# Performance work log

Measured on AMD Instinct MI355X. Metric: run time of the kernel, lower is better.

Reference implementation:

```python
import jax, jax.numpy as jnp
import numpy as np

B, N, E = 2, 10000, 80000
NODE_DIM, EDGE_DIM = 30, 3
H, VE, EE = 64, 16, 16  # encoder_hidden_dim -> width AND depth of hidden chain


def _mlp_params(key, din, h, dout, prefix):
    k = jax.random.split(key, 6)
    s_in, s_h = 1.0 / np.sqrt(din), 1.0 / np.sqrt(h)
    return {
        prefix + '_Win': jax.random.normal(k[0], (din, h), jnp.float32) * s_in,
        prefix + '_bin': jax.random.normal(k[1], (h,), jnp.float32) * s_in,
        prefix + '_Whid': jax.random.normal(k[2], (h, h, h), jnp.float32) * s_h,  # h stacked hidden Linears
        prefix + '_bhid': jax.random.normal(k[3], (h, h), jnp.float32) * s_h,
        prefix + '_Wout': jax.random.normal(k[4], (h, dout), jnp.float32) * s_h,
        prefix + '_bout': jax.random.normal(k[5], (dout,), jnp.float32) * s_h,
    }


def setup_inputs() -> dict:
    key = jax.random.key(0)
    ks = jax.random.split(key, 8)
    inp = {
        'nodes': jax.random.normal(ks[0], (B, N, NODE_DIM), jnp.float32),
        'globals_': jax.random.normal(ks[1], (B,), jnp.float32),
        'edges': jax.random.normal(ks[2], (B, E, EDGE_DIM), jnp.float32),
        'senders': jax.random.randint(ks[3], (B, E), 0, N, jnp.int32),
        'receivers': jax.random.randint(ks[4], (B, E), 0, N, jnp.int32),
    }
    inp.update(_mlp_params(ks[5], NODE_DIM + 1, H, VE, 'node'))  # +1 global col
    inp.update(_mlp_params(ks[6], EDGE_DIM + 4, H, EE, 'edge'))  # +4 relative feats
    return inp


def _chain(x, Win, b_in, Whid, bhid, Wout, bout):
    # Linear(in,h) -> h x Linear(h,h) -> Linear(h,out); NO nonlinearity (matches source)
    h = x @ Win + b_in
    def step(c, wb):
        W, b = wb
        return c @ W + b, None
    h, _ = jax.lax.scan(step, h, (Whid, bhid))
    return h @ Wout + bout


def reference(nodes, globals_, edges, senders, receivers,
              node_Win, node_bin, node_Whid, node_bhid, node_Wout, node_bout,
              edge_Win, edge_bin, edge_Whid, edge_bhid, edge_Wout, edge_bout):
    Bv, Nv = nodes.shape[0], nodes.shape[1]
    g = jnp.broadcast_to(globals_[:, None, None], (Bv, Nv, 1))
    nodes_g = jnp.concatenate([nodes, g], axis=-1)  # [B,N,node_dim+1]
    pos = nodes_g[..., :3]  # first 3 features are 3D positions
    gather = jax.vmap(lambda p, idx: p[idx])
    s = gather(pos, senders)    # [B,E,3]
    r = gather(pos, receivers)  # [B,E,3]
    d = s - r
    norm = jnp.linalg.norm(d, axis=-1, keepdims=True)
    edges_full = jnp.concatenate([edges, d, norm], axis=-1)  # [B,E,edge_dim+4]
    latent_nodes = _chain(nodes_g, node_Win, node_bin, node_Whid, node_bhid, node_Wout, node_bout)
    latent_edges = _chain(edges_full, edge_Win, edge_bin, edge_Whid, edge_bhid, edge_Wout, edge_bout)
    return latent_nodes, latent_edges
```

## Files before the change

### kernel.cpp

```cpp
#include <hip/hip_runtime.h>

typedef unsigned int uint32;

#define NN 10000
#define EE_ 80000
#define NODE_ROWS 20000
#define NODE_BLOCKS 79
#define EDGE_BLOCKS 625

#define FLAG_MAGIC 0x5EEDF00Du
#define FLAG_BASE_U32 640

typedef float f4 __attribute__((ext_vector_type(4)));

#define GLD4(g, l) __builtin_amdgcn_global_load_lds(                      \
    (const __attribute__((address_space(1))) void*)(g),                   \
    (__attribute__((address_space(3))) void*)(l), 16, 0, 0)
#define GLD1(g, l) __builtin_amdgcn_global_load_lds(                      \
    (const __attribute__((address_space(1))) void*)(g),                   \
    (__attribute__((address_space(3))) void*)(l), 4, 0, 0)

__global__ __launch_bounds__(256, 1) void collapse_kernel(
    const float* __restrict__ nWin, const float* __restrict__ nbin,
    const float* __restrict__ nWhid, const float* __restrict__ nbhid,
    const float* __restrict__ nWout, const float* __restrict__ nbout,
    const float* __restrict__ eWin, const float* __restrict__ ebin,
    const float* __restrict__ eWhid, const float* __restrict__ ebhid,
    const float* __restrict__ eWout, const float* __restrict__ ebout,
    float* __restrict__ ws)
{
  __shared__ float smem[13312];
  const int t = threadIdx.x;
  const int c  = blockIdx.x >> 4;
  const int jq = blockIdx.x & 15;
  float* pt = ws + 1024;
  uint32* ws_u = (uint32*)ws;

  {
    float* s_at = smem;
    float* s_b  = smem + 8704;
    float* s_bp = smem + 12864;
    const float* Wh = c ? eWhid : nWhid;
    const float* bh = c ? ebhid : nbhid;
    const int L0 = 4*jq;

    for (int idx = t; idx < 4160; idx += 256) {
      int r = idx >> 6, k = idx & 63;
      s_at[k*68 + r] = (r < 64) ? Wh[(size_t)L0*4096 + idx] : bh[L0*64 + k];
    }
    int cur = 0;
    #pragma unroll 1
    for (int s = 1; s <= 3; ++s) {
      const float* WB = Wh + (size_t)(L0 + s)*4096;
      const float* bB = bh + (size_t)(L0 + s)*64;
      #pragma unroll
      for (int i = 0; i < 4; ++i) {
        int i4 = t + i*256;
        *(float4*)&s_b[i4*4] = *(const float4*)&WB[i4*4];
      }
      if (t < 16) *(float4*)&s_b[4096 + t*4] = *(const float4*)&bB[t*4];
      __syncthreads();

      const int ti = t >> 4, tj = t & 15;
      float acc[4][4];
      #pragma unroll
      for (int d = 0; d < 4; ++d)
        #pragma unroll
        for (int e = 0; e < 4; ++e) acc[d][e] = 0.f;
      #pragma unroll 4
      for (int k = 0; k < 64; ++k) {
        float4 a4 = *(const float4*)&s_at[cur*4352 + k*68 + 4*ti];
        float4 b4 = *(const float4*)&s_b[k*64 + 4*tj];
        float av[4] = {a4.x, a4.y, a4.z, a4.w};
        float bv[4] = {b4.x, b4.y, b4.z, b4.w};
        #pragma unroll
        for (int d = 0; d < 4; ++d)
          #pragma unroll
          for (int e = 0; e < 4; ++e) acc[d][e] += av[d]*bv[e];
      }
      {
        int cc = t & 63, kq = t >> 6;
        float p = 0.f;
        #pragma unroll 4
        for (int kk = 0; kk < 16; ++kk) {
          int k = kq*16 + kk;
          p += s_at[cur*4352 + k*68 + 64] * s_b[k*64 + cc];
        }
        s_bp[kq*64 + cc] = p;
      }
      __syncthreads();
      if (s < 3) {
        #pragma unroll
        for (int d = 0; d < 4; ++d)
          #pragma unroll
          for (int e = 0; e < 4; ++e)
            s_at[(cur^1)*4352 + (4*tj + e)*68 + 4*ti + d] = acc[d][e];
        if (t < 64)
          s_at[(cur^1)*4352 + t*68 + 64] =
              s_bp[t] + s_bp[64+t] + s_bp[128+t] + s_bp[192+t] + s_b[4096+t];
        __syncthreads();
        cur ^= 1;
      } else {
        float* D = pt + (size_t)(c*16 + jq)*4160;
        #pragma unroll
        for (int d = 0; d < 4; ++d)
          *(float4*)&D[(4*ti + d)*64 + 4*tj] =
              make_float4(acc[d][0], acc[d][1], acc[d][2], acc[d][3]);
        if (t < 64)
          D[4096 + t] = s_bp[t] + s_bp[64+t] + s_bp[128+t] + s_bp[192+t] + s_b[4096+t];
      }
    }
  }

  __syncthreads();
  if (t == 0) {
    __threadfence();
    __hip_atomic_store(ws_u + FLAG_BASE_U32 + (c*16 + jq)*8, FLAG_MAGIC,
                       __ATOMIC_RELEASE, __HIP_MEMORY_SCOPE_AGENT);
  }
  if (t < 16) {
    const uint32* p = ws_u + FLAG_BASE_U32 + (c*16 + t)*8;
    int guard = 0;
    while (__hip_atomic_load(p, __ATOMIC_ACQUIRE, __HIP_MEMORY_SCOPE_AGENT)
           != FLAG_MAGIC) {
      __builtin_amdgcn_s_sleep(2);
      if (++guard > (1 << 20)) break;
    }
  }
  __syncthreads();

  {
    float* lds_f = smem;
    const int lane = t & 63;
    const int wv   = __builtin_amdgcn_readfirstlane(t >> 6);
    const int q = jq;
    const float* Win  = c ? eWin  : nWin;
    const float* bin  = c ? ebin  : nbin;
    const float* Wout = c ? eWout : nWout;
    const float* bout = c ? ebout : nbout;
    const float* PT = pt + (size_t)c*16*4160;
    const int din = c ? 7 : 31;
    float* weff = ws + (c ? 512 : 0);

    const int r4 = lane >> 4, c16 = lane & 15;
    const int oE = r4*64 + ((c16 ^ r4) << 2);
    const int oO = r4*64 + ((c16 ^ (4 | r4)) << 2);
    const int swz = lane & 7;
    const int aw0 = lane*256 + (((4*wv + 0) ^ swz) << 4);
    const int aw1 = lane*256 + (((4*wv + 1) ^ swz) << 4);
    const int aw2 = lane*256 + (((4*wv + 2) ^ swz) << 4);
    const int aw3 = lane*256 + (((4*wv + 3) ^ swz) << 4);
    const int ab  = 16384 + wv*256 + lane*4;
    const int apw = 52224 + lane*16 + wv*4;
    const int apr = 52224 + lane*16;

    float vlane = Wout[lane*16 + q];
    float bpart = 0.f;
    const int kbase = 16*wv;
    float s[16];
    #pragma unroll
    for (int j = 0; j < 16; ++j)
      s[j] = __uint_as_float(__builtin_amdgcn_readlane(__float_as_uint(vlane), kbase + j));

#define STAGE(BF, L) do {                                                 \
    const float* gW_ = PT + (size_t)(L)*4160 + wv*1024;                   \
    float* lW_ = lds_f + (BF)*4352 + wv*1024;                             \
    GLD4(gW_ +   0 + oE, lW_ +   0);                                      \
    GLD4(gW_ + 256 + oO, lW_ + 256);                                      \
    GLD4(gW_ + 512 + oE, lW_ + 512);                                      \
    GLD4(gW_ + 768 + oO, lW_ + 768);                                      \
    GLD1(PT + (size_t)(L)*4160 + 4096 + lane,                             \
         lds_f + (BF)*4352 + 4096 + wv*64);                               \
  } while (0)

#define CSTEP(OFS, VMC, STAGESTMT) do {                                   \
    STAGESTMT;                                                            \
    asm volatile("s_waitcnt vmcnt(" #VMC ") lgkmcnt(0)" ::: "memory");    \
    __builtin_amdgcn_s_barrier();                                         \
    f4 f0_, f1_, f2_, f3_; float bb_;                                     \
    asm volatile("ds_read_b128 %0, %5 offset:" #OFS "\n\t"                \
                 "ds_read_b128 %1, %6 offset:" #OFS "\n\t"                \
                 "ds_read_b128 %2, %7 offset:" #OFS "\n\t"                \
                 "ds_read_b128 %3, %8 offset:" #OFS "\n\t"                \
                 "ds_read_b32  %4, %9 offset:" #OFS "\n\t"                \
                 "s_waitcnt lgkmcnt(0)"                                   \
                 : "=&v"(f0_), "=&v"(f1_), "=&v"(f2_), "=&v"(f3_), "=&v"(bb_) \
                 : "v"(aw0), "v"(aw1), "v"(aw2), "v"(aw3), "v"(ab)        \
                 : "memory");                                             \
    __builtin_amdgcn_sched_barrier(0);                                    \
    bpart = __builtin_fmaf(bb_, vlane, bpart);                            \
    float a0_ = __builtin_fmaf(f0_.y, s[1],  f0_.x * s[0]);               \
    a0_ = __builtin_fmaf(f0_.z, s[2],  a0_);                              \
    a0_ = __builtin_fmaf(f0_.w, s[3],  a0_);                              \
    float a1_ = __builtin_fmaf(f1_.y, s[5],  f1_.x * s[4]);               \
    a1_ = __builtin_fmaf(f1_.z, s[6],  a1_);                              \
    a1_ = __builtin_fmaf(f1_.w, s[7],  a1_);                              \
    float a2_ = __builtin_fmaf(f2_.y, s[9],  f2_.x * s[8]);               \
    a2_ = __builtin_fmaf(f2_.z, s[10], a2_);                              \
    a2_ = __builtin_fmaf(f2_.w, s[11], a2_);                              \
    float a3_ = __builtin_fmaf(f3_.y, s[13], f3_.x * s[12]);              \
    a3_ = __builtin_fmaf(f3_.z, s[14], a3_);                              \
    a3_ = __builtin_fmaf(f3_.w, s[15], a3_);                              \
    float acc_ = (a0_ + a1_) + (a2_ + a3_);                               \
    asm volatile("ds_write_b32 %0, %1\n\t"                                \
                 "s_waitcnt lgkmcnt(0)"                                   \
                 :: "v"(apw), "v"(acc_) : "memory");                      \
    __builtin_amdgcn_s_barrier();                                         \
    f4 p4_;                                                               \
    asm volatile("ds_read_b128 %0, %1\n\t"                                \
                 "s_waitcnt lgkmcnt(0)"                                   \
                 : "=&v"(p4_) : "v"(apr) : "memory");                     \
    __builtin_amdgcn_sched_barrier(0);                                    \
    vlane = (p4_.x + p4_.y) + (p4_.z + p4_.w);                            \
    _Pragma("unroll")                                                     \
    for (int jj = 0; jj < 16; ++jj)                                       \
      s[jj] = __uint_as_float(__builtin_amdgcn_readlane(                  \
                  __float_as_uint(vlane), kbase + jj));                   \
  } while (0)

    STAGE(0, 15);
    STAGE(1, 14);

    int L = 15;
    #pragma unroll 1
    for (int ii = 0; ii < 4; ++ii) {
      CSTEP(0,     10, STAGE(2, L-2));
      CSTEP(17408, 10, STAGE(0, L-3));
      CSTEP(34816, 10, STAGE(1, L-4));
      L -= 3;
    }
    CSTEP(0,     10, STAGE(2, 1));
    CSTEP(17408, 10, STAGE(0, 0));
    CSTEP(34816, 5,  (void)0);
    CSTEP(0,     0,  (void)0);
#undef CSTEP
#undef STAGE

    if (wv != 0) return;

    float red = __builtin_fmaf(bin[lane], vlane, bpart);
    #pragma unroll
    for (int off = 32; off > 0; off >>= 1) red += __shfl_xor(red, off, 64);

    float* sv = lds_f;
    sv[lane] = vlane;
    __builtin_amdgcn_sched_barrier(0);

    if (lane == din) {
      weff[din*16 + q] = red + bout[q];
    } else if (lane < din) {
      float a0 = 0.f, a1 = 0.f, a2 = 0.f, a3 = 0.f;
      const float* wr = Win + (size_t)lane*64;
      #pragma unroll
      for (int kb = 0; kb < 16; ++kb) {
        f4 vv = *(const f4*)&sv[kb*4];
        f4 wv4 = *(const f4*)&wr[kb*4];
        a0 = __builtin_fmaf(wv4.x, vv.x, a0);
        a1 = __builtin_fmaf(wv4.y, vv.y, a1);
        a2 = __builtin_fmaf(wv4.z, vv.z, a2);
        a3 = __builtin_fmaf(wv4.w, vv.w, a3);
      }
      weff[lane*16 + q] = (a0 + a1) + (a2 + a3);
    }
  }
}

template<int NF>
static __device__ __forceinline__ void mlp_apply_store(const float* x, const float* sW,
                                                       float* po)
{
  float a[16];
  #pragma unroll
  for (int q = 0; q < 16; ++q) a[q] = sW[NF*16 + q];
  #pragma unroll
  for (int j = 0; j < NF; ++j) {
    const float xv = x[j];
    #pragma unroll
    for (int q = 0; q < 16; ++q) a[q] += xv * sW[j*16 + q];
  }
  float4* d = (float4*)po;
  d[0] = make_float4(a[0],  a[1],  a[2],  a[3]);
  d[1] = make_float4(a[4],  a[5],  a[6],  a[7]);
  d[2] = make_float4(a[8],  a[9],  a[10], a[11]);
  d[3] = make_float4(a[12], a[13], a[14], a[15]);
}

__global__ __launch_bounds__(256) void apply_kernel(
    const float* __restrict__ nodes, const float* __restrict__ globals_,
    const float* __restrict__ edges, const int* __restrict__ senders,
    const int* __restrict__ receivers, const float* __restrict__ ws,
    float* __restrict__ out)
{
  __shared__ float sW[32*16];
  const bool is_node = (blockIdx.x < NODE_BLOCKS);
  {
    const float* src = is_node ? ws : ws + 512;
    const int n = is_node ? 32*16 : 8*16;
    for (int j = threadIdx.x; j < n; j += 256) sW[j] = src[j];
  }
  __syncthreads();

  if (is_node) {
    const int rn = blockIdx.x*256 + threadIdx.x;
    if (rn >= NODE_ROWS) return;
    float x[31];
    const float* p = nodes + (size_t)rn*30;
    #pragma unroll
    for (int j = 0; j < 15; ++j) {
      float2 u = *(const float2*)(p + j*2);
      x[2*j]     = u.x;
      x[2*j + 1] = u.y;
    }
    const int b = (rn >= NN) ? 1 : 0;
    x[30] = globals_[b];
    mlp_apply_store<31>(x, sW, out + (size_t)rn*16);
  } else {
    const int re = (blockIdx.x - NODE_BLOCKS)*256 + threadIdx.x;
    const int b = (re >= EE_) ? 1 : 0;
    float x[7];
    const float* ep = edges + (size_t)re*3;
    x[0] = ep[0]; x[1] = ep[1]; x[2] = ep[2];
    const int si = senders[re], ri = receivers[re];
    const float* ps = nodes + ((size_t)(b*NN + si))*30;
    const float* pr = nodes + ((size_t)(b*NN + ri))*30;
    const float dx = ps[0] - pr[0];
    const float dy = ps[1] - pr[1];
    const float dz = ps[2] - pr[2];
    x[3] = dx; x[4] = dy; x[5] = dz;
    x[6] = sqrtf(dx*dx + dy*dy + dz*dz);
    mlp_apply_store<7>(x, sW, out + (size_t)(NODE_ROWS + re)*16);
  }
}

extern "C" void kernel_launch(void* const* d_in, const int* in_sizes, int n_in,
                              void* d_out, int out_size, void* d_ws, size_t ws_size,
                              hipStream_t stream)
{
  const float* nodes    = (const float*)d_in[0];
  const float* globals_ = (const float*)d_in[1];
  const float* edges    = (const float*)d_in[2];
  const int* senders   = (const int*)d_in[3];
  const int* receivers = (const int*)d_in[4];
  const float* nWin  = (const float*)d_in[5];
  const float* nbin  = (const float*)d_in[6];
  const float* nWhid = (const float*)d_in[7];
  const float* nbhid = (const float*)d_in[8];
  const float* nWout = (const float*)d_in[9];
  const float* nbout = (const float*)d_in[10];
  const float* eWin  = (const float*)d_in[11];
  const float* ebin  = (const float*)d_in[12];
  const float* eWhid = (const float*)d_in[13];
  const float* ebhid = (const float*)d_in[14];
  const float* eWout = (const float*)d_in[15];
  const float* ebout = (const float*)d_in[16];
  float* ws  = (float*)d_ws;
  float* out = (float*)d_out;

  collapse_kernel<<<32, 256, 0, stream>>>(
      nWin, nbin, nWhid, nbhid, nWout, nbout,
      eWin, ebin, eWhid, ebhid, eWout, ebout, ws);

  apply_kernel<<<NODE_BLOCKS + EDGE_BLOCKS, 256, 0, stream>>>(
      nodes, globals_, edges, senders, receivers, ws, out);
}
```

Baseline: 37.63 us.

## Fuse weight-collapse and apply kernels into one flag-synchronized mega kernel

Merges the collapse and apply kernels into a single launch. The first 32 blocks compute the collapsed effective weights and publish per-column and per-chain ready flags. The remaining blocks load their node and edge inputs, including the sender/receiver gathers, before spin-waiting on the flag for their chain. This removes the second launch and its gap, and overlaps input fetching with the weight collapse. In exchange it relies on all blocks being co-resident, since the apply blocks now use the large shared allocation. The flags are never reset, so on repeated calls the apply blocks may not wait and could read weights that are still being rewritten.

```diff
diff --git a/kernel.cpp b/kernel.cpp
--- a/kernel.cpp
+++ b/kernel.cpp
@@ -7,9 +7,14 @@
 #define NODE_ROWS 20000
 #define NODE_BLOCKS 79
 #define EDGE_BLOCKS 625
+#define COLLAPSE_BLOCKS 32
+#define TOTAL_BLOCKS (COLLAPSE_BLOCKS + NODE_BLOCKS + EDGE_BLOCKS)
 
 #define FLAG_MAGIC 0x5EEDF00Du
-#define FLAG_BASE_U32 640
+#define CHUNKFLAG_U32 640
+#define COLFLAG_U32   960
+#define CHAINFLAG_U32 1280
+#define PT_F 2048
 
 typedef float f4 __attribute__((ext_vector_type(4)));
 
@@ -20,21 +25,107 @@
     (const __attribute__((address_space(1))) void*)(g),                   \
     (__attribute__((address_space(3))) void*)(l), 4, 0, 0)
 
-__global__ __launch_bounds__(256, 1) void collapse_kernel(
+template<int NF>
+static __device__ __forceinline__ void mlp_apply_store(const float* x, const float* sW,
+                                                       float* po)
+{
+  float a[16];
+  #pragma unroll
+  for (int q = 0; q < 16; ++q) a[q] = sW[NF*16 + q];
+  #pragma unroll
+  for (int j = 0; j < NF; ++j) {
+    const float xv = x[j];
+    #pragma unroll
+    for (int q = 0; q < 16; ++q) a[q] += xv * sW[j*16 + q];
+  }
+  float4* d = (float4*)po;
+  d[0] = make_float4(a[0],  a[1],  a[2],  a[3]);
+  d[1] = make_float4(a[4],  a[5],  a[6],  a[7]);
+  d[2] = make_float4(a[8],  a[9],  a[10], a[11]);
+  d[3] = make_float4(a[12], a[13], a[14], a[15]);
+}
+
+__global__ __launch_bounds__(256, 1) void mega_kernel(
+    const float* __restrict__ nodes, const float* __restrict__ globals_,
+    const float* __restrict__ edges, const int* __restrict__ senders,
+    const int* __restrict__ receivers,
     const float* __restrict__ nWin, const float* __restrict__ nbin,
     const float* __restrict__ nWhid, const float* __restrict__ nbhid,
     const float* __restrict__ nWout, const float* __restrict__ nbout,
     const float* __restrict__ eWin, const float* __restrict__ ebin,
     const float* __restrict__ eWhid, const float* __restrict__ ebhid,
     const float* __restrict__ eWout, const float* __restrict__ ebout,
-    float* __restrict__ ws)
+    float* __restrict__ ws, float* __restrict__ out)
 {
   __shared__ float smem[13312];
   const int t = threadIdx.x;
+  uint32* ws_u = (uint32*)ws;
+  float* pt = ws + PT_F;
+
+  if (blockIdx.x >= COLLAPSE_BLOCKS) {
+    const int ab = blockIdx.x - COLLAPSE_BLOCKS;
+    const bool is_node = (ab < NODE_BLOCKS);
+    float x[31];
+    int rn = 0, re = 0, b = 0;
+    bool active = true;
+    if (is_node) {
+      rn = ab*256 + t;
+      active = (rn < NODE_ROWS);
+      if (active) {
+        const float* p = nodes + (size_t)rn*30;
+        #pragma unroll
+        for (int j = 0; j < 15; ++j) {
+          float2 u = *(const float2*)(p + j*2);
+          x[2*j]     = u.x;
+          x[2*j + 1] = u.y;
+        }
+        b = (rn >= NN) ? 1 : 0;
+        x[30] = globals_[b];
+      }
+    } else {
+      re = (ab - NODE_BLOCKS)*256 + t;
+      b = (re >= EE_) ? 1 : 0;
+      const float* ep = edges + (size_t)re*3;
+      x[0] = ep[0]; x[1] = ep[1]; x[2] = ep[2];
+      const int si = senders[re], ri = receivers[re];
+      const float* ps = nodes + ((size_t)(b*NN + si))*30;
+      const float* pr = nodes + ((size_t)(b*NN + ri))*30;
+      const float dx = ps[0] - pr[0];
+      const float dy = ps[1] - pr[1];
+      const float dz = ps[2] - pr[2];
+      x[3] = dx; x[4] = dy; x[5] = dz;
+      x[6] = sqrtf(dx*dx + dy*dy + dz*dz);
+    }
+    if (active) {
+      const int nf = is_node ? 31 : 7;
+      #pragma unroll
+      for (int i = 0; i < 31; ++i)
+        if (i < nf) asm volatile("" :: "v"(x[i]));
+    }
+    if (t == 0) {
+      const uint32* p = ws_u + CHAINFLAG_U32 + (is_node ? 0 : 8);
+      int guard = 0;
+      while (__hip_atomic_load(p, __ATOMIC_ACQUIRE, __HIP_MEMORY_SCOPE_AGENT)
+             != FLAG_MAGIC) {
+        __builtin_amdgcn_s_sleep(32);
+        if (++guard > (1 << 16)) break;
+      }
+    }
+    __syncthreads();
+    {
+      const float* src = ws + (is_node ? 0 : 512);
+      const int n = is_node ? 512 : 128;
+      for (int j = t; j < n; j += 256) smem[j] = src[j];
+    }
+    __syncthreads();
+    if (!active) return;
+    if (is_node) mlp_apply_store<31>(x, smem, out + (size_t)rn*16);
+    else         mlp_apply_store<7>(x, smem, out + (size_t)(NODE_ROWS + re)*16);
+    return;
+  }
+
   const int c  = blockIdx.x >> 4;
   const int jq = blockIdx.x & 15;
-  float* pt = ws + 1024;
-  uint32* ws_u = (uint32*)ws;
 
   {
     float* s_at = smem;
@@ -79,14 +170,14 @@
           for (int e = 0; e < 4; ++e) acc[d][e] += av[d]*bv[e];
       }
       {
-        int cc = t & 63, kq = t >> 6;
+        int cc2 = t & 63, kq = t >> 6;
         float p = 0.f;
         #pragma unroll 4
         for (int kk = 0; kk < 16; ++kk) {
           int k = kq*16 + kk;
-          p += s_at[cur*4352 + k*68 + 64] * s_b[k*64 + cc];
+          p += s_at[cur*4352 + k*68 + 64] * s_b[k*64 + cc2];
         }
-        s_bp[kq*64 + cc] = p;
+        s_bp[kq*64 + cc2] = p;
       }
       __syncthreads();
       if (s < 3) {
@@ -115,11 +206,11 @@
   __syncthreads();
   if (t == 0) {
     __threadfence();
-    __hip_atomic_store(ws_u + FLAG_BASE_U32 + (c*16 + jq)*8, FLAG_MAGIC,
+    __hip_atomic_store(ws_u + CHUNKFLAG_U32 + (c*16 + jq)*8, FLAG_MAGIC,
                        __ATOMIC_RELEASE, __HIP_MEMORY_SCOPE_AGENT);
   }
   if (t < 16) {
-    const uint32* p = ws_u + FLAG_BASE_U32 + (c*16 + t)*8;
+    const uint32* p = ws_u + CHUNKFLAG_U32 + (c*16 + t)*8;
     int guard = 0;
     while (__hip_atomic_load(p, __ATOMIC_ACQUIRE, __HIP_MEMORY_SCOPE_AGENT)
            != FLAG_MAGIC) {
@@ -150,7 +241,7 @@
     const int aw1 = lane*256 + (((4*wv + 1) ^ swz) << 4);
     const int aw2 = lane*256 + (((4*wv + 2) ^ swz) << 4);
     const int aw3 = lane*256 + (((4*wv + 3) ^ swz) << 4);
-    const int ab  = 16384 + wv*256 + lane*4;
+    const int ab2 = 16384 + wv*256 + lane*4;
     const int apw = 52224 + lane*16 + wv*4;
     const int apr = 52224 + lane*16;
 
@@ -185,7 +276,7 @@
                  "ds_read_b32  %4, %9 offset:" #OFS "\n\t"                \
                  "s_waitcnt lgkmcnt(0)"                                   \
                  : "=&v"(f0_), "=&v"(f1_), "=&v"(f2_), "=&v"(f3_), "=&v"(bb_) \
-                 : "v"(aw0), "v"(aw1), "v"(aw2), "v"(aw3), "v"(ab)        \
+                 : "v"(aw0), "v"(aw1), "v"(aw2), "v"(aw3), "v"(ab2)       \
                  : "memory");                                             \
     __builtin_amdgcn_sched_barrier(0);                                    \
     bpart = __builtin_fmaf(bb_, vlane, bpart);                            \
@@ -262,73 +353,25 @@
       }
       weff[lane*16 + q] = (a0 + a1) + (a2 + a3);
     }
-  }
-}
-
-template<int NF>
-static __device__ __forceinline__ void mlp_apply_store(const float* x, const float* sW,
-                                                       float* po)
-{
-  float a[16];
-  #pragma unroll
-  for (int q = 0; q < 16; ++q) a[q] = sW[NF*16 + q];
-  #pragma unroll
-  for (int j = 0; j < NF; ++j) {
-    const float xv = x[j];
-    #pragma unroll
-    for (int q = 0; q < 16; ++q) a[q] += xv * sW[j*16 + q];
-  }
-  float4* d = (float4*)po;
-  d[0] = make_float4(a[0],  a[1],  a[2],  a[3]);
-  d[1] = make_float4(a[4],  a[5],  a[6],  a[7]);
-  d[2] = make_float4(a[8],  a[9],  a[10], a[11]);
-  d[3] = make_float4(a[12], a[13], a[14], a[15]);
-}
-
-__global__ __launch_bounds__(256) void apply_kernel(
-    const float* __restrict__ nodes, const float* __restrict__ globals_,
-    const float* __restrict__ edges, const int* __restrict__ senders,
-    const int* __restrict__ receivers, const float* __restrict__ ws,
-    float* __restrict__ out)
-{
-  __shared__ float sW[32*16];
-  const bool is_node = (blockIdx.x < NODE_BLOCKS);
-  {
-    const float* src = is_node ? ws : ws + 512;
-    const int n = is_node ? 32*16 : 8*16;
-    for (int j = threadIdx.x; j < n; j += 256) sW[j] = src[j];
-  }
-  __syncthreads();
-
-  if (is_node) {
-    const int rn = blockIdx.x*256 + threadIdx.x;
-    if (rn >= NODE_ROWS) return;
-    float x[31];
-    const float* p = nodes + (size_t)rn*30;
-    #pragma unroll
-    for (int j = 0; j < 15; ++j) {
-      float2 u = *(const float2*)(p + j*2);
-      x[2*j]     = u.x;
-      x[2*j + 1] = u.y;
-    }
-    const int b = (rn >= NN) ? 1 : 0;
-    x[30] = globals_[b];
-    mlp_apply_store<31>(x, sW, out + (size_t)rn*16);
-  } else {
-    const int re = (blockIdx.x - NODE_BLOCKS)*256 + threadIdx.x;
-    const int b = (re >= EE_) ? 1 : 0;
-    float x[7];
-    const float* ep = edges + (size_t)re*3;
-    x[0] = ep[0]; x[1] = ep[1]; x[2] = ep[2];
-    const int si = senders[re], ri = receivers[re];
-    const float* ps = nodes + ((size_t)(b*NN + si))*30;
-    const float* pr = nodes + ((size_t)(b*NN + ri))*30;
-    const float dx = ps[0] - pr[0];
-    const float dy = ps[1] - pr[1];
-    const float dz = ps[2] - pr[2];
-    x[3] = dx; x[4] = dy; x[5] = dz;
-    x[6] = sqrtf(dx*dx + dy*dy + dz*dz);
-    mlp_apply_store<7>(x, sW, out + (size_t)(NODE_ROWS + re)*16);
+
+    __threadfence();
+    if (lane == 0)
+      __hip_atomic_store(ws_u + COLFLAG_U32 + (c*16 + q)*8, FLAG_MAGIC,
+                         __ATOMIC_RELEASE, __HIP_MEMORY_SCOPE_AGENT);
+    if (q == 0) {
+      if (lane < 16) {
+        const uint32* p = ws_u + COLFLAG_U32 + (c*16 + lane)*8;
+        int guard = 0;
+        while (__hip_atomic_load(p, __ATOMIC_ACQUIRE, __HIP_MEMORY_SCOPE_AGENT)
+               != FLAG_MAGIC) {
+          __builtin_amdgcn_s_sleep(2);
+          if (++guard > (1 << 20)) break;
+        }
+      }
+      if (lane == 0)
+        __hip_atomic_store(ws_u + CHAINFLAG_U32 + c*8, FLAG_MAGIC,
+                           __ATOMIC_RELEASE, __HIP_MEMORY_SCOPE_AGENT);
+    }
   }
 }
 
@@ -356,10 +399,8 @@
   float* ws  = (float*)d_ws;
   float* out = (float*)d_out;
 
-  collapse_kernel<<<32, 256, 0, stream>>>(
+  mega_kernel<<<TOTAL_BLOCKS, 256, 0, stream>>>(
+      nodes, globals_, edges, senders, receivers,
       nWin, nbin, nWhid, nbhid, nWout, nbout,
-      eWin, ebin, eWhid, ebhid, eWout, ebout, ws);
-
-  apply_kernel<<<NODE_BLOCKS + EDGE_BLOCKS, 256, 0, stream>>>(
-      nodes, globals_, edges, senders, receivers, ws, out);
+      eWin, ebin, eWhid, ebhid, eWout, ebout, ws, out);
 }
```

New measurement: 128.9 us. 243% more time.
